# Performance work log

Hardware: AMD Instinct MI355X
Metric: run time of the kernel (lower is better)

Reference implementation:

```python
import jax, jax.numpy as jnp
import numpy as np

N_NODES = 100000


def _gcn_norm(edge_index, edge_weight, n):
    # add self-loops with weight 1 (PyG gcn_norm default fill_value=1.0)
    row = jnp.concatenate([edge_index[0], jnp.arange(n, dtype=edge_index.dtype)])
    col = jnp.concatenate([edge_index[1], jnp.arange(n, dtype=edge_index.dtype)])
    w = jnp.concatenate([edge_weight, jnp.ones((n,), dtype=edge_weight.dtype)])
    deg = jax.ops.segment_sum(w, col, num_segments=n)
    dinv = jnp.where(deg > 0, jax.lax.rsqrt(jnp.where(deg > 0, deg, 1.0)), 0.0)
    norm = dinv[row] * w * dinv[col]  # [E+N]
    return row, col, norm


def _gcn_conv(x, row, col, norm, W, b, n):
    h = x @ W                                   # [N, out] dense projection first (in > out)
    msg = norm[:, None] * h[row]                # gather + scale
    out = jax.ops.segment_sum(msg, col, num_segments=n)  # scatter-add to targets
    return out + b


def setup_inputs() -> dict:
    key = jax.random.key(0)
    ks = jax.random.split(key, 6)
    n, e, f, h, c = N_NODES, 3200000, 256, 64, 40
    return {
        "x": jax.random.normal(ks[0], (n, f), dtype=jnp.float32),
        "edge_index": jax.random.randint(ks[1], (2, e), 0, n, dtype=jnp.int64),
        "edge_weight": jax.random.uniform(ks[2], (e,), dtype=jnp.float32),
        "W1": jax.random.normal(ks[3], (f, h), dtype=jnp.float32) / np.sqrt(f),
        "b1": jnp.zeros((h,), dtype=jnp.float32),
        "W2": jax.random.normal(ks[4], (h, c), dtype=jnp.float32) / np.sqrt(h),
        "b2": jnp.zeros((c,), dtype=jnp.float32),
    }


def reference(x, edge_index, edge_weight, W1, b1, W2, b2):
    n = x.shape[0]
    row, col, norm = _gcn_norm(edge_index, edge_weight, n)
    # layer 1: GCNConv -> identity activation -> dropout (identity at eval)
    h = _gcn_conv(x, row, col, norm, W1, b1, n)
    # layer 2: GCNConv (classifier head)
    out = _gcn_conv(h, row, col, norm, W2, b2, n)
    return out
```

## Files before the change

### kernel.cpp

```cpp
#include <hip/hip_runtime.h>
#include <hip/hip_fp16.h>
#include <cstdint>
#include <cstddef>


#define TB 256
#define NBK 200
#define LCAP 32
#define SPLIT 4

typedef _Float16 half8 __attribute__((ext_vector_type(8)));
typedef float f32x4 __attribute__((ext_vector_type(4)));

__global__ void k_detect(const unsigned* ei, int* flag) {
    int t = threadIdx.x;
    unsigned v = 0;
    for (int i = t; i < 256; i += 64) v |= ei[2 * i + 1];
    unsigned long long any = __ballot(v != 0u);
    if (t == 0) *flag = (any != 0ull) ? 1 : 0;
}

__global__ void k_zero(int* p, int n) {
    int i = blockIdx.x * blockDim.x + threadIdx.x;
    if (i < n) p[i] = 0;
}

__global__ __launch_bounds__(256) void k_binA(const void* __restrict__ ei,
                                              const int* __restrict__ flag,
                                              const float* __restrict__ ew,
                                              int* __restrict__ tail,
                                              int2* __restrict__ stage,
                                              int per, int E, int capb) {
    __shared__ int2 lbuf[NBK][LCAP];
    __shared__ int lcnt[NBK];
    int t = threadIdx.x;
    for (int i = t; i < NBK; i += 256) lcnt[i] = 0;
    __syncthreads();
    int s0 = blockIdx.x * per;
    int s1 = min(E, s0 + per);
    int isI32 = *flag;
    const int* p32 = (const int*)ei;
    const long long* p64 = (const long long*)ei;
    for (int b0 = s0; b0 < s1; b0 += 2048) {
        int2 ent[8];
        int bk[8];
#pragma unroll
        for (int u = 0; u < 8; u++) {
            int e = b0 + u * 256 + t;
            bk[u] = -1;
            if (e < s1) {
                int r, c;
                if (isI32) { r = p32[e]; c = p32[E + e]; }
                else       { r = (int)p64[e]; c = (int)p64[E + e]; }
                bk[u] = c >> 9;
                ent[u] = make_int2((r << 9) | (c & 511), __float_as_int(ew[e]));
            }
        }
#pragma unroll
        for (int u = 0; u < 8; u++) {
            if (bk[u] < 0) continue;
            int pos = atomicAdd(&lcnt[bk[u]], 1);
            if (pos < LCAP) {
                lbuf[bk[u]][pos] = ent[u];
            } else {
                int g = atomicAdd(&tail[bk[u]], 1);
                if (g < capb) stage[(size_t)bk[u] * capb + g] = ent[u];
            }
        }
        __syncthreads();
        if (t < NBK) {
            int c = min(lcnt[t], LCAP);
            int n16 = c & ~15;
            if (n16) {
                int base = atomicAdd(&tail[t], n16);
                size_t db = (size_t)t * capb;
                for (int j = 0; j < n16; j++) {
                    int g = base + j;
                    if (g < capb) stage[db + g] = lbuf[t][j];
                }
                int rem = c - n16;
                for (int j = 0; j < rem; j++) lbuf[t][j] = lbuf[t][n16 + j];
                lcnt[t] = rem;
            } else {
                lcnt[t] = c;
            }
        }
        __syncthreads();
    }
    if (t < NBK) {
        int c = min(lcnt[t], LCAP);
        if (c) {
            int base = atomicAdd(&tail[t], c);
            size_t db = (size_t)t * capb;
            for (int j = 0; j < c; j++) {
                int g = base + j;
                if (g < capb) stage[db + g] = lbuf[t][j];
            }
        }
    }
}

__global__ void k_bscan(const int* __restrict__ tail, int* __restrict__ bbase,
                        int* __restrict__ ptr2, int nbk, int capb, int N) {
    __shared__ int sm[256];
    int t = threadIdx.x;
    int v = (t < nbk) ? min(tail[t], capb) : 0;
    sm[t] = v;
    __syncthreads();
    for (int off = 1; off < 256; off <<= 1) {
        int add = (t >= off) ? sm[t - off] : 0;
        __syncthreads();
        sm[t] += add;
        __syncthreads();
    }
    if (t < nbk) bbase[t] = sm[t] - v;
    if (t == nbk - 1) ptr2[(size_t)N * 4] = sm[t];
}

__global__ __launch_bounds__(512) void k_binB(const int* __restrict__ tail,
                                              const int* __restrict__ bbase,
                                              const int2* __restrict__ stage,
                                              int2* __restrict__ csr,
                                              int* __restrict__ ptr2,
                                              float* __restrict__ dinv,
                                              int N, int capb, int qn) {
    __shared__ int h2[2048];
    __shared__ float wsm[512];
    __shared__ int sm[512];
    __shared__ int lpos2[2048];
    int b = blockIdx.x, t = threadIdx.x;
    for (int i = t; i < 2048; i += 512) h2[i] = 0;
    wsm[t] = 0.f;
    __syncthreads();
    int tot = min(tail[b], capb);
    size_t sb = (size_t)b * capb;
    for (int j = t; j < tot; j += 512) {
        int2 v = stage[sb + j];
        int cl = v.x & 511;
        int src = v.x >> 9;
        int rng = min(src / qn, SPLIT - 1);
        atomicAdd(&h2[(cl << 2) | rng], 1);
        atomicAdd(&wsm[cl], __int_as_float(v.y));
    }
    __syncthreads();
    int a0 = h2[t * 4], a1 = h2[t * 4 + 1], a2 = h2[t * 4 + 2], a3 = h2[t * 4 + 3];
    int s = a0 + a1 + a2 + a3;
    sm[t] = s;
    __syncthreads();
    for (int off = 1; off < 512; off <<= 1) {
        int add = (t >= off) ? sm[t - off] : 0;
        __syncthreads();
        sm[t] += add;
        __syncthreads();
    }
    int ex = sm[t] - s;
    int base = bbase[b];
    int node = b * 512 + t;
    int e0 = ex, e1 = ex + a0, e2 = e1 + a1, e3 = e2 + a2;
    if (node < N) {
        ptr2[(size_t)node * 4 + 0] = base + e0;
        ptr2[(size_t)node * 4 + 1] = base + e1;
        ptr2[(size_t)node * 4 + 2] = base + e2;
        ptr2[(size_t)node * 4 + 3] = base + e3;
        dinv[node] = rsqrtf(1.0f + wsm[t]);
    }
    lpos2[t * 4 + 0] = e0;
    lpos2[t * 4 + 1] = e1;
    lpos2[t * 4 + 2] = e2;
    lpos2[t * 4 + 3] = e3;
    __syncthreads();
    for (int j = t; j < tot; j += 512) {
        int2 v = stage[sb + j];
        int cl = v.x & 511;
        int src = v.x >> 9;
        int rng = min(src / qn, SPLIT - 1);
        int idx = atomicAdd(&lpos2[(cl << 2) | rng], 1);
        csr[base + idx] = make_int2(src, v.y);
    }
}

__global__ void k_wc(const float* __restrict__ W1, const float* __restrict__ b1,
                     const float* __restrict__ W2, __half* __restrict__ Wcf,
                     float* __restrict__ bw) {
    __shared__ float w2s[64 * 40];
    __shared__ __half wcs[256][40];
    int t = threadIdx.x;
    for (int i = t; i < 64 * 40; i += 256) w2s[i] = W2[i];
    __syncthreads();
    float acc[40];
#pragma unroll
    for (int j = 0; j < 40; j++) acc[j] = 0.f;
    for (int k = 0; k < 64; k++) {
        float a = W1[t * 64 + k];
#pragma unroll
        for (int j = 0; j < 40; j++) acc[j] = fmaf(a, w2s[k * 40 + j], acc[j]);
    }
    for (int j = 0; j < 40; j++) wcs[t][j] = __float2half(acc[j]);
    if (t < 40) {
        float accb = 0.f;
        for (int k = 0; k < 64; k++) accb = fmaf(b1[k], w2s[k * 40 + t], accb);
        bw[t] = accb;
    }
    __syncthreads();
    for (int s = 0; s < 48; s++) {
        int o = t * 48 + s;
        int j = o & 7;
        int lane = (o >> 3) & 63;
        int f = o >> 9;
        int nt = f % 3, kt = f / 3;
        int k = kt * 32 + (lane >> 4) * 8 + j;
        int c = nt * 16 + (lane & 15);
        Wcf[o] = (c < 40) ? wcs[k][c] : __float2half(0.f);
    }
}

__global__ __launch_bounds__(256, 2) void k_zmm(const float* __restrict__ x,
                                                const __half* __restrict__ Wcf,
                                                __half* __restrict__ Zh, int n) {
    __shared__ __align__(16) unsigned char xs[128 * 64 * 2];
    int t = threadIdx.x;
    int w = t >> 6;
    int l = t & 63;
    int rlo = l & 15;
    int khi = l >> 4;
    int row0 = blockIdx.x * 128;
    f32x4 acc[2][3];
#pragma unroll
    for (int m = 0; m < 2; m++)
#pragma unroll
        for (int nt = 0; nt < 3; nt++) acc[m][nt] = (f32x4){0.f, 0.f, 0.f, 0.f};

    for (int k0 = 0; k0 < 256; k0 += 64) {
        __syncthreads();
#pragma unroll
        for (int s = 0; s < 8; s++) {
            int i = t + 256 * s;
            int rr = i >> 4;
            int kq = (i & 15) * 4;
            int grow = min(row0 + rr, n - 1);
            float4 v = *(const float4*)&x[(size_t)grow * 256 + k0 + kq];
            __half2 h01 = __floats2half2_rn(v.x, v.y);
            __half2 h23 = __floats2half2_rn(v.z, v.w);
            float2 pk;
            ((__half2*)&pk)[0] = h01;
            ((__half2*)&pk)[1] = h23;
            int byte = (rr * 128 + kq * 2) ^ ((rr & 7) << 4);
            *(float2*)(xs + byte) = pk;
        }
        __syncthreads();
        half8 bfr[2][3];
#pragma unroll
        for (int kt2 = 0; kt2 < 2; kt2++)
#pragma unroll
            for (int nt = 0; nt < 3; nt++) {
                int f = (k0 / 32 + kt2) * 3 + nt;
                bfr[kt2][nt] = *(const half8*)&Wcf[(size_t)(f * 64 + l) * 8];
            }
#pragma unroll
        for (int kt2 = 0; kt2 < 2; kt2++) {
#pragma unroll
            for (int m = 0; m < 2; m++) {
                int row = (w * 2 + m) * 16 + rlo;
                int byte = (row * 128 + kt2 * 64 + khi * 16) ^ ((row & 7) << 4);
                half8 af = *(const half8*)(xs + byte);
#pragma unroll
                for (int nt = 0; nt < 3; nt++)
                    acc[m][nt] = __builtin_amdgcn_mfma_f32_16x16x32_f16(af, bfr[kt2][nt], acc[m][nt], 0, 0, 0);
            }
        }
    }
#pragma unroll
    for (int m = 0; m < 2; m++) {
#pragma unroll
        for (int nt = 0; nt < 3; nt++) {
            int col = nt * 16 + rlo;
            if (col < 40) {
#pragma unroll
                for (int reg = 0; reg < 4; reg++) {
                    int grow = row0 + (w * 2 + m) * 16 + khi * 4 + reg;
                    if (grow < n) Zh[(size_t)grow * 40 + col] = __float2half(acc[m][nt][reg]);
                }
            }
        }
    }
}

__device__ inline float4 ldh4(const __half* p) {
    float2 raw = *(const float2*)p;
    const __half2* h = (const __half2*)&raw;
    float2 a = __half22float2(h[0]);
    float2 b = __half22float2(h[1]);
    return make_float4(a.x, a.y, b.x, b.y);
}

template <int MODE>
__global__ __launch_bounds__(320) void k_gather(const int* __restrict__ ptr2,
                                                const int2* __restrict__ csr,
                                                const __half* __restrict__ src,
                                                const float* __restrict__ dinv,
                                                const float* __restrict__ bw,
                                                const float* __restrict__ b2,
                                                __half* __restrict__ dsth,
                                                float* __restrict__ dstf, int n) {
    int t = threadIdx.x;
    int ln = t / 10;
    int node = blockIdx.x * 32 + ln;
    if (node >= n) return;
    int q = t - ln * 10;
    int c0 = q * 4;
    float d = dinv[node];
    float d2 = d * d;
    const float4 zs = ldh4(&src[(size_t)node * 40 + c0]);
    float ax = d2 * zs.x, ay = d2 * zs.y, az = d2 * zs.z, aw = d2 * zs.w;
    float sw = 0.f;
    int p[SPLIT + 1];
#pragma unroll
    for (int h = 0; h <= SPLIT; h++) p[h] = ptr2[(size_t)node * 4 + h];
#pragma unroll
    for (int h = 0; h < SPLIT; h++) {
#pragma unroll 4
        for (int j = p[h]; j < p[h + 1]; j++) {
            int2 e = csr[j];
            int r = e.x;
            float nv = dinv[r] * __int_as_float(e.y) * d;
            const float4 zv = ldh4(&src[(size_t)r * 40 + c0]);
            if (MODE) sw += nv;
            ax = fmaf(nv, zv.x, ax);
            ay = fmaf(nv, zv.y, ay);
            az = fmaf(nv, zv.z, az);
            aw = fmaf(nv, zv.w, aw);
        }
    }
    if (MODE) {
        float sb = sw + d2;
        ax += sb * bw[c0 + 0] + b2[c0 + 0];
        ay += sb * bw[c0 + 1] + b2[c0 + 1];
        az += sb * bw[c0 + 2] + b2[c0 + 2];
        aw += sb * bw[c0 + 3] + b2[c0 + 3];
        float4 o;
        o.x = ax; o.y = ay; o.z = az; o.w = aw;
        *(float4*)&dstf[(size_t)node * 40 + c0] = o;
    } else {
        __half2 h0 = __floats2half2_rn(ax, ay);
        __half2 h1 = __floats2half2_rn(az, aw);
        float2 packed;
        ((__half2*)&packed)[0] = h0;
        ((__half2*)&packed)[1] = h1;
        *(float2*)&dsth[(size_t)node * 40 + c0] = packed;
    }
}

extern "C" void kernel_launch(void* const* d_in, const int* in_sizes, int n_in,
                              void* d_out, int out_size, void* d_ws, size_t ws_size,
                              hipStream_t stream) {
    const float* x  = (const float*)d_in[0];
    const void*  ei = d_in[1];
    const float* ew = (const float*)d_in[2];
    const float* W1 = (const float*)d_in[3];
    const float* b1 = (const float*)d_in[4];
    const float* W2 = (const float*)d_in[5];
    const float* b2 = (const float*)d_in[6];
    float* out = (float*)d_out;

    const int E = in_sizes[1] / 2;
    const int N = in_sizes[0] / 256;
    const int nbk = (N + 511) >> 9;
    const int capb = E / nbk + 2048;
    const int qn = (N + SPLIT - 1) / SPLIT;

    char* ws = (char*)d_ws;
    float*  dinv = (float*)(ws + 0);
    int*    flag = (int*)(ws + (1u << 19));
    float*  bw   = (float*)(ws + (1u << 19) + 256);
    __half* Wcf  = (__half*)(ws + (1u << 19) + 4096);
    int*    tail = (int*)(ws + (1u << 19) + 65536);
    int*    bbase = (int*)(ws + (1u << 19) + 65536 + 4096);
    size_t off = (size_t)1 << 20;
    size_t estride = ((size_t)E * 4 + 255) & ~(size_t)255;
    size_t n4stride = ((size_t)(N * 4 + 1) * 4 + 255) & ~(size_t)255;
    size_t hstride = ((size_t)N * 40 * 2 + 255) & ~(size_t)255;
    int*    ptr2 = (int*)(ws + off);    off += n4stride;
    int2*   csr  = (int2*)(ws + off);   off += 2 * estride;
    int2*   stage = (int2*)(ws + off);  off += (size_t)NBK * capb * 8;
    __half* Zh   = (__half*)(ws + off); off += hstride;
    __half* T1h  = (__half*)(ws + off);

    const int NB = 608;
    const int per = (E + NB - 1) / NB;
    int gb = (N + 31) / 32;

    k_detect<<<1, 64, 0, stream>>>((const unsigned*)ei, flag);
    k_zero<<<1, NBK, 0, stream>>>(tail, NBK);
    k_binA<<<NB, 256, 0, stream>>>(ei, flag, ew, tail, stage, per, E, capb);
    k_bscan<<<1, 256, 0, stream>>>(tail, bbase, ptr2, nbk, capb, N);
    k_binB<<<nbk, 512, 0, stream>>>(tail, bbase, stage, csr, ptr2, dinv, N, capb, qn);
    k_wc<<<1, TB, 0, stream>>>(W1, b1, W2, Wcf, bw);
    k_zmm<<<(N + 127) / 128, TB, 0, stream>>>(x, Wcf, Zh, N);
    k_gather<0><<<gb, 320, 0, stream>>>(ptr2, csr, Zh, dinv, bw, b2, T1h, nullptr, N);
    k_gather<1><<<gb, 320, 0, stream>>>(ptr2, csr, T1h, dinv, bw, b2, nullptr, out, N);
}
```

Before: 311.6 us.

## Stage block CSR edges with pre-scaled weights in LDS; widen gather to 8 cols

The gather kernel now handles 64 nodes per block, with 5 threads per node each covering 8 fp16 columns through 16-byte loads. The block's contiguous CSR edge range is loaded cooperatively into shared memory in chunks, and the dinv[src]*weight product is computed once per edge during staging. This replaces the per-thread dinv lookups and the 4-way split pointer walk. The goal is fewer global loads per edge, and the cost is extra __syncthreads plus the assumption that ptr2[node*4] indexes a contiguous per-node range.

After: 290.7 us. -6.7%, faster.

```diff
diff --git a/kernel.cpp b/kernel.cpp
--- a/kernel.cpp
+++ b/kernel.cpp
@@ -8,6 +8,7 @@
 #define NBK 200
 #define LCAP 32
 #define SPLIT 4
+#define GCAP 2048
 
 typedef _Float16 half8 __attribute__((ext_vector_type(8)));
 typedef float f32x4 __attribute__((ext_vector_type(4)));
@@ -285,14 +286,6 @@
     }
 }
 
-__device__ inline float4 ldh4(const __half* p) {
-    float2 raw = *(const float2*)p;
-    const __half2* h = (const __half2*)&raw;
-    float2 a = __half22float2(h[0]);
-    float2 b = __half22float2(h[1]);
-    return make_float4(a.x, a.y, b.x, b.y);
-}
-
 template <int MODE>
 __global__ __launch_bounds__(320) void k_gather(const int* __restrict__ ptr2,
                                                 const int2* __restrict__ csr,
@@ -302,51 +295,82 @@
                                                 const float* __restrict__ b2,
                                                 __half* __restrict__ dsth,
                                                 float* __restrict__ dstf, int n) {
-    int t = threadIdx.x;
-    int ln = t / 10;
-    int node = blockIdx.x * 32 + ln;
-    if (node >= n) return;
-    int q = t - ln * 10;
-    int c0 = q * 4;
-    float d = dinv[node];
-    float d2 = d * d;
-    const float4 zs = ldh4(&src[(size_t)node * 40 + c0]);
-    float ax = d2 * zs.x, ay = d2 * zs.y, az = d2 * zs.z, aw = d2 * zs.w;
+    __shared__ int2 se[GCAP];
+    int t = threadIdx.x;
+    int ln = t / 5;
+    int q = t - ln * 5;
+    int c0 = q * 8;
+    int n0 = blockIdx.x * 64;
+    int node = n0 + ln;
+    int n1 = min(n0 + 64, n);
+    int st0 = ptr2[(size_t)n0 * 4];
+    int en0 = ptr2[(size_t)n1 * 4];
+    bool act = (node < n1);
+    float d = 0.f, d2 = 0.f;
+    int st = 0, en = 0;
+    float a0 = 0.f, a1 = 0.f, a2 = 0.f, a3 = 0.f, a4 = 0.f, a5 = 0.f, a6 = 0.f, a7 = 0.f;
     float sw = 0.f;
-    int p[SPLIT + 1];
-#pragma unroll
-    for (int h = 0; h <= SPLIT; h++) p[h] = ptr2[(size_t)node * 4 + h];
-#pragma unroll
-    for (int h = 0; h < SPLIT; h++) {
+    if (act) {
+        d = dinv[node];
+        d2 = d * d;
+        st = ptr2[(size_t)node * 4];
+        en = ptr2[(size_t)(node + 1) * 4];
+        float4 raw = *(const float4*)&src[(size_t)node * 40 + c0];
+        const __half2* hh = (const __half2*)&raw;
+        float2 f0 = __half22float2(hh[0]), f1 = __half22float2(hh[1]);
+        float2 f2 = __half22float2(hh[2]), f3 = __half22float2(hh[3]);
+        a0 = d2 * f0.x; a1 = d2 * f0.y; a2 = d2 * f1.x; a3 = d2 * f1.y;
+        a4 = d2 * f2.x; a5 = d2 * f2.y; a6 = d2 * f3.x; a7 = d2 * f3.y;
+    }
+    for (int base = st0; base < en0; base += GCAP) {
+        int m = min(GCAP, en0 - base);
+        __syncthreads();
+        for (int i = t; i < m; i += 320) {
+            int2 e = csr[base + i];
+            se[i] = make_int2(e.x, __float_as_int(dinv[e.x] * __int_as_float(e.y)));
+        }
+        __syncthreads();
+        if (act) {
+            int lo = max(st, base) - base;
+            int hi = min(en, base + m) - base;
 #pragma unroll 4
-        for (int j = p[h]; j < p[h + 1]; j++) {
-            int2 e = csr[j];
-            int r = e.x;
-            float nv = dinv[r] * __int_as_float(e.y) * d;
-            const float4 zv = ldh4(&src[(size_t)r * 40 + c0]);
-            if (MODE) sw += nv;
-            ax = fmaf(nv, zv.x, ax);
-            ay = fmaf(nv, zv.y, ay);
-            az = fmaf(nv, zv.z, az);
-            aw = fmaf(nv, zv.w, aw);
-        }
-    }
+            for (int j = lo; j < hi; j++) {
+                int2 e = se[j];
+                float nv = __int_as_float(e.y) * d;
+                float4 raw = *(const float4*)&src[(size_t)e.x * 40 + c0];
+                const __half2* hh = (const __half2*)&raw;
+                float2 f0 = __half22float2(hh[0]), f1 = __half22float2(hh[1]);
+                float2 f2 = __half22float2(hh[2]), f3 = __half22float2(hh[3]);
+                if (MODE) sw += nv;
+                a0 = fmaf(nv, f0.x, a0); a1 = fmaf(nv, f0.y, a1);
+                a2 = fmaf(nv, f1.x, a2); a3 = fmaf(nv, f1.y, a3);
+                a4 = fmaf(nv, f2.x, a4); a5 = fmaf(nv, f2.y, a5);
+                a6 = fmaf(nv, f3.x, a6); a7 = fmaf(nv, f3.y, a7);
+            }
+        }
+    }
+    if (!act) return;
     if (MODE) {
         float sb = sw + d2;
-        ax += sb * bw[c0 + 0] + b2[c0 + 0];
-        ay += sb * bw[c0 + 1] + b2[c0 + 1];
-        az += sb * bw[c0 + 2] + b2[c0 + 2];
-        aw += sb * bw[c0 + 3] + b2[c0 + 3];
-        float4 o;
-        o.x = ax; o.y = ay; o.z = az; o.w = aw;
-        *(float4*)&dstf[(size_t)node * 40 + c0] = o;
+        a0 += sb * bw[c0 + 0] + b2[c0 + 0];
+        a1 += sb * bw[c0 + 1] + b2[c0 + 1];
+        a2 += sb * bw[c0 + 2] + b2[c0 + 2];
+        a3 += sb * bw[c0 + 3] + b2[c0 + 3];
+        a4 += sb * bw[c0 + 4] + b2[c0 + 4];
+        a5 += sb * bw[c0 + 5] + b2[c0 + 5];
+        a6 += sb * bw[c0 + 6] + b2[c0 + 6];
+        a7 += sb * bw[c0 + 7] + b2[c0 + 7];
+        float4 o0 = make_float4(a0, a1, a2, a3);
+        float4 o1 = make_float4(a4, a5, a6, a7);
+        *(float4*)&dstf[(size_t)node * 40 + c0] = o0;
+        *(float4*)&dstf[(size_t)node * 40 + c0 + 4] = o1;
     } else {
-        __half2 h0 = __floats2half2_rn(ax, ay);
-        __half2 h1 = __floats2half2_rn(az, aw);
-        float2 packed;
-        ((__half2*)&packed)[0] = h0;
-        ((__half2*)&packed)[1] = h1;
-        *(float2*)&dsth[(size_t)node * 40 + c0] = packed;
+        float4 packed;
+        ((__half2*)&packed)[0] = __floats2half2_rn(a0, a1);
+        ((__half2*)&packed)[1] = __floats2half2_rn(a2, a3);
+        ((__half2*)&packed)[2] = __floats2half2_rn(a4, a5);
+        ((__half2*)&packed)[3] = __floats2half2_rn(a6, a7);
+        *(float4*)&dsth[(size_t)node * 40 + c0] = packed;
     }
 }
 
@@ -387,7 +411,7 @@
 
     const int NB = 608;
     const int per = (E + NB - 1) / NB;
-    int gb = (N + 31) / 32;
+    int gb = (N + 63) / 64;
 
     k_detect<<<1, 64, 0, stream>>>((const unsigned*)ei, flag);
     k_zero<<<1, NBK, 0, stream>>>(tail, NBK);
```
